# Kernel optimization log

Measured on AMD Instinct MI355X. Metric: run time of the kernel, lower is better.

## Reference

```python
import jax, jax.numpy as jnp
import numpy as np

H, DI, N, K, R, FF = 2048, 4096, 16, 4, 128, 5632
B, S = 2, 1024
EPS = 1e-6


def rmsnorm(x, w):
    v = jnp.mean(x * x, axis=-1, keepdims=True)
    return x * jax.lax.rsqrt(v + EPS) * w


def setup_inputs() -> dict:
    key = jax.random.key(0)
    ks = jax.random.split(key, 16)
    sc = 0.02
    inp = {
        "hidden_states": jax.random.normal(ks[0], (B, S, H), jnp.float32),
        "input_ln_w": jnp.ones((H,), jnp.float32),
        "w_in": jax.random.normal(ks[1], (2 * DI, H), jnp.float32) * sc,
        "conv_w": jax.random.normal(ks[2], (DI, 1, K), jnp.float32) * 0.3,
        "conv_b": jax.random.normal(ks[3], (DI,), jnp.float32) * sc,
        "w_x": jax.random.normal(ks[4], (R + 2 * N, DI), jnp.float32) * sc,
        "dt_ln_w": jnp.ones((R,), jnp.float32),
        "b_ln_w": jnp.ones((N,), jnp.float32),
        "c_ln_w": jnp.ones((N,), jnp.float32),
        "w_dt": jax.random.normal(ks[5], (DI, R), jnp.float32) * sc,
        "b_dt": jax.random.normal(ks[6], (DI,), jnp.float32) * sc - 4.0,
        "A_log": jnp.broadcast_to(jnp.log(jnp.arange(1, N + 1, dtype=jnp.float32)), (DI, N)),
        "D_skip": jnp.ones((DI,), jnp.float32),
        "w_out": jax.random.normal(ks[7], (H, DI), jnp.float32) * sc,
        "pre_ff_ln_w": jnp.ones((H,), jnp.float32),
        "w_gate": jax.random.normal(ks[8], (FF, H), jnp.float32) * sc,
        "w_up": jax.random.normal(ks[9], (FF, H), jnp.float32) * sc,
        "w_down": jax.random.normal(ks[10], (H, FF), jnp.float32) * sc,
    }
    return inp


def causal_conv1d(x, w, b):
    # x: [B,S,DI], w: [DI,1,K] depthwise, left-pad K-1 (causal)
    y = jax.lax.conv_general_dilated(
        x.transpose(0, 2, 1), w,
        window_strides=(1,), padding=[(K - 1, 0)],
        dimension_numbers=("NCH", "OIH", "NCH"),
        feature_group_count=DI)
    return (y + b[None, :, None]).transpose(0, 2, 1)


def selective_scan(u, A, Bm, Cm, Dp, dt):
    # u,dt: [B,S,DI]; A: [DI,N]; Bm,Cm: [B,S,N]
    def step(h, xs):
        dt_t, B_t, C_t, u_t = xs  # [B,DI],[B,N],[B,N],[B,DI]
        dA = jnp.exp(dt_t[:, :, None] * A)                      # [B,DI,N]
        dBu = dt_t[:, :, None] * B_t[:, None, :] * u_t[:, :, None]
        h = dA * h + dBu
        y = jnp.einsum("bdn,bn->bd", h, C_t)
        return h, y

    xs = (dt.transpose(1, 0, 2), Bm.transpose(1, 0, 2),
          Cm.transpose(1, 0, 2), u.transpose(1, 0, 2))
    h0 = jnp.zeros((u.shape[0], DI, N), u.dtype)
    _, ys = jax.lax.scan(step, h0, xs)
    return ys.transpose(1, 0, 2) + u * Dp  # [B,S,DI]


def reference(hidden_states, input_ln_w, w_in, conv_w, conv_b, w_x, dt_ln_w,
              b_ln_w, c_ln_w, w_dt, b_dt, A_log, D_skip, w_out, pre_ff_ln_w,
              w_gate, w_up, w_down):
    residual = hidden_states
    x = rmsnorm(hidden_states, input_ln_w)

    # --- Mamba mixer ---
    proj = x @ w_in.T                       # [B,S,2*DI]
    u, gate = jnp.split(proj, 2, axis=-1)
    u = jax.nn.silu(causal_conv1d(u, conv_w, conv_b))
    ssm_p = u @ w_x.T                       # [B,S,R+2N]
    t_r, Bm, Cm = jnp.split(ssm_p, [R, R + N], axis=-1)
    t_r = rmsnorm(t_r, dt_ln_w)
    Bm = rmsnorm(Bm, b_ln_w)
    Cm = rmsnorm(Cm, c_ln_w)
    dt = jax.nn.softplus(t_r @ w_dt.T + b_dt)  # [B,S,DI]
    A = -jnp.exp(A_log)
    y = selective_scan(u, A, Bm, Cm, D_skip, dt)
    y = y * jax.nn.silu(gate)
    mixer_out = y @ w_out.T                  # [B,S,H]

    hidden = residual + mixer_out
    residual = hidden
    h = rmsnorm(hidden, pre_ff_ln_w)
    ff = (jax.nn.silu(h @ w_gate.T) * (h @ w_up.T)) @ w_down.T
    return residual + ff
```

## Files before the change

### kernel.cpp

```cpp
#include <hip/hip_runtime.h>
#include <stdint.h>

#define H_   2048
#define DI_  4096
#define N_   16
#define K_   4
#define R_   128
#define FF_  5632
#define B_   2
#define S_   1024
#define MROWS (B_*S_)
#define PCH  32
#define CSTEPS (S_/PCH)

typedef float f32x4 __attribute__((ext_vector_type(4)));
typedef float f32x2 __attribute__((ext_vector_type(2)));
typedef __bf16 bf16x8 __attribute__((ext_vector_type(8)));

#define LOG2E 1.4426950408889634f
#define LN2   0.6931471805599453f

__device__ __forceinline__ unsigned short f2bf(float f) {
    union { float f; unsigned u; } v; v.f = f;
    unsigned r = v.u + 0x7fffu + ((v.u >> 16) & 1u);
    return (unsigned short)(r >> 16);
}

__device__ __forceinline__ float bf2f(unsigned short u) {
    union { unsigned u; float f; } v; v.u = ((unsigned)u) << 16;
    return v.f;
}

__device__ __forceinline__ float fexp2(float x) { return __builtin_amdgcn_exp2f(x); }
__device__ __forceinline__ float flog2(float x) { return __builtin_amdgcn_logf(x); }

__device__ __forceinline__ float softplus2(float v) {
    return (v > 20.f) ? v : LN2 * flog2(1.f + fexp2(v * LOG2E));
}

__device__ __forceinline__ void gload16(const void* g, void* lds) {
    __builtin_amdgcn_global_load_lds(
        (const __attribute__((address_space(1))) unsigned int*)(uintptr_t)g,
        (__attribute__((address_space(3))) unsigned int*)(unsigned int)(uintptr_t)lds,
        16, 0, 0);
}

__global__ __launch_bounds__(256, 2)
void gemm_bt(const unsigned short* __restrict__ A, const unsigned short* __restrict__ Bt,
             void* __restrict__ Cv, int M, int N, int K, int Kc, int obf)
{
    __shared__ __align__(16) unsigned short As[128 * 64];
    __shared__ __align__(16) unsigned short Bs[128 * 64];
    const int t = threadIdx.x;
    const int l = t & 63;
    const int wv = t >> 6;

    int nwg = gridDim.x * gridDim.y;
    int wg = blockIdx.y * gridDim.x + blockIdx.x;
    if ((nwg & 7) == 0) {
        int q = nwg >> 3;
        wg = (wg & 7) * q + (wg >> 3);
    }
    const int bx = wg / gridDim.y;
    const int by = wg % gridDim.y;
    const long m0 = (long)by * 128;
    const long n0 = (long)bx * 128;
    const int wm = (wv >> 1) * 64;
    const int wn = (wv & 1) * 64;
    const long kstart = (long)blockIdx.z * Kc;
    const long cbase = (long)blockIdx.z * M * (long)N;

    f32x4 acc[4][4] = {};

    const int tr = t >> 3;
    const int cs = (t & 7) ^ (tr & 7);
    const unsigned short* gA = A + (m0 + tr) * (long)K + kstart + cs * 8;
    const unsigned short* gB = Bt + (n0 + tr) * (long)K + kstart + cs * 8;
    const unsigned ldsbase = (unsigned)(t & 192) * 16;

    for (int kt = 0; kt < Kc; kt += 64) {
#pragma unroll
        for (int j = 0; j < 4; ++j) {
            gload16(gA + (long)j * 32 * K, (char*)As + j * 4096 + ldsbase);
            gload16(gB + (long)j * 32 * K, (char*)Bs + j * 4096 + ldsbase);
        }
        gA += 64; gB += 64;
        __syncthreads();
#pragma unroll
        for (int k0 = 0; k0 < 2; ++k0) {
            bf16x8 af[4], bfr[4];
#pragma unroll
            for (int i = 0; i < 4; ++i) {
                int rowa = wm + i * 16 + (l & 15);
                int ca = (k0 * 4 + (l >> 4)) ^ (rowa & 7);
                af[i] = *(const bf16x8*)(As + rowa * 64 + ca * 8);
                int rowb = wn + i * 16 + (l & 15);
                int cb = (k0 * 4 + (l >> 4)) ^ (rowb & 7);
                bfr[i] = *(const bf16x8*)(Bs + rowb * 64 + cb * 8);
            }
#pragma unroll
            for (int i = 0; i < 4; ++i)
#pragma unroll
                for (int jn = 0; jn < 4; ++jn)
                    acc[i][jn] = __builtin_amdgcn_mfma_f32_16x16x32_bf16(
                        af[i], bfr[jn], acc[i][jn], 0, 0, 0);
        }
        __syncthreads();
    }

    const int crow = (l >> 4) * 4;
    const int ccol = l & 15;
    float* Cf = (float*)Cv + cbase;
    unsigned short* Cb = (unsigned short*)Cv + cbase;
#pragma unroll
    for (int i = 0; i < 4; ++i) {
#pragma unroll
        for (int jn = 0; jn < 4; ++jn) {
            long row = m0 + wm + i * 16 + crow;
            long col = n0 + wn + jn * 16 + ccol;
            if (obf) {
                unsigned short* cp = Cb + row * (long)N + col;
#pragma unroll
                for (int q = 0; q < 4; ++q) cp[(long)q * N] = f2bf(acc[i][jn][q]);
            } else {
                float* cp = Cf + row * (long)N + col;
#pragma unroll
                for (int q = 0; q < 4; ++q) cp[(long)q * N] = acc[i][jn][q];
            }
        }
    }
}

__global__ __launch_bounds__(512, 1)
void gemm_bt256(const unsigned short* __restrict__ A, const unsigned short* __restrict__ Bt,
                void* __restrict__ Cv, int M, int N, int K, int Kc, int obf)
{
    __shared__ __align__(16) unsigned short As[2][256 * 64];
    __shared__ __align__(16) unsigned short Bs[2][256 * 64];
    const int t = threadIdx.x;
    const int l = t & 63;
    const int wv = t >> 6;
    const int wm = wv >> 2;
    const int wn = wv & 3;

    int nwg = gridDim.x * gridDim.y;
    int wg = blockIdx.y * gridDim.x + blockIdx.x;
    if ((nwg & 7) == 0) {
        int q = nwg >> 3;
        wg = (wg & 7) * q + (wg >> 3);
    }
    const int bx = wg / gridDim.y;
    const int by = wg % gridDim.y;
    const long m0 = (long)by * 256;
    const long n0 = (long)bx * 256;
    const long kstart = (long)blockIdx.z * Kc;
    const long cbase = (long)blockIdx.z * M * (long)N;

    f32x4 acc[8][4] = {};

    const int cs = (t & 7) ^ ((t >> 3) & 7);
    const unsigned short* gA = A + (m0 + (t >> 3)) * (long)K + kstart + cs * 8;
    const unsigned short* gB = Bt + (n0 + (t >> 3)) * (long)K + kstart + cs * 8;
    const int NT = Kc >> 6;

#pragma unroll
    for (int i = 0; i < 4; ++i)
        gload16(gA + (long)i * 64 * K, &As[0][t * 8 + i * 4096]);
#pragma unroll
    for (int i = 0; i < 4; ++i)
        gload16(gB + (long)i * 64 * K, &Bs[0][t * 8 + i * 4096]);

    for (int kt = 0; kt < NT; ++kt) {
        const int buf = kt & 1;
        const long koff = (long)((kt + 1 < NT) ? (kt + 1) : kt) * 64;
#pragma unroll
        for (int i = 0; i < 4; ++i)
            gload16(gA + koff + (long)i * 64 * K, &As[buf ^ 1][t * 8 + i * 4096]);
        asm volatile("s_waitcnt vmcnt(4)" ::: "memory");
        __builtin_amdgcn_sched_barrier(0);
        __builtin_amdgcn_s_barrier();
        __builtin_amdgcn_sched_barrier(0);
        {
            bf16x8 af[8], bfr[4];
#pragma unroll
            for (int nf = 0; nf < 4; ++nf) {
                int rowb = wn * 64 + nf * 16 + (l & 15);
                int cb = (l >> 4) ^ (rowb & 7);
                bfr[nf] = *(const bf16x8*)(&Bs[buf][rowb * 64 + cb * 8]);
            }
#pragma unroll
            for (int mf = 0; mf < 8; ++mf) {
                int rowa = wm * 128 + mf * 16 + (l & 15);
                int ca = (l >> 4) ^ (rowa & 7);
                af[mf] = *(const bf16x8*)(&As[buf][rowa * 64 + ca * 8]);
            }
            __builtin_amdgcn_s_setprio(1);
#pragma unroll
            for (int mf = 0; mf < 8; ++mf)
#pragma unroll
                for (int nf = 0; nf < 4; ++nf)
                    acc[mf][nf] = __builtin_amdgcn_mfma_f32_16x16x32_bf16(
                        af[mf], bfr[nf], acc[mf][nf], 0, 0, 0);
            __builtin_amdgcn_s_setprio(0);
        }
        __builtin_amdgcn_sched_barrier(0);
#pragma unroll
        for (int i = 0; i < 4; ++i)
            gload16(gB + koff + (long)i * 64 * K, &Bs[buf ^ 1][t * 8 + i * 4096]);
        {
            bf16x8 af[8], bfr[4];
#pragma unroll
            for (int nf = 0; nf < 4; ++nf) {
                int rowb = wn * 64 + nf * 16 + (l & 15);
                int cb = (4 + (l >> 4)) ^ (rowb & 7);
                bfr[nf] = *(const bf16x8*)(&Bs[buf][rowb * 64 + cb * 8]);
            }
#pragma unroll
            for (int mf = 0; mf < 8; ++mf) {
                int rowa = wm * 128 + mf * 16 + (l & 15);
                int ca = (4 + (l >> 4)) ^ (rowa & 7);
                af[mf] = *(const bf16x8*)(&As[buf][rowa * 64 + ca * 8]);
            }
            __builtin_amdgcn_s_setprio(1);
#pragma unroll
            for (int mf = 0; mf < 8; ++mf)
#pragma unroll
                for (int nf = 0; nf < 4; ++nf)
                    acc[mf][nf] = __builtin_amdgcn_mfma_f32_16x16x32_bf16(
                        af[mf], bfr[nf], acc[mf][nf], 0, 0, 0);
            __builtin_amdgcn_s_setprio(0);
        }
        __builtin_amdgcn_sched_barrier(0);
        __builtin_amdgcn_s_barrier();
        __builtin_amdgcn_sched_barrier(0);
    }

    const int crow = (l >> 4) * 4;
    const int ccol = l & 15;
    float* Cf = (float*)Cv + cbase;
    unsigned short* Cb = (unsigned short*)Cv + cbase;
#pragma unroll
    for (int mf = 0; mf < 8; ++mf) {
#pragma unroll
        for (int nf = 0; nf < 4; ++nf) {
            long row = m0 + wm * 128 + mf * 16 + crow;
            long col = n0 + wn * 64 + nf * 16 + ccol;
            if (obf) {
                unsigned short* cp = Cb + row * (long)N + col;
#pragma unroll
                for (int q = 0; q < 4; ++q) cp[(long)q * N] = f2bf(acc[mf][nf][q]);
            } else {
                float* cp = Cf + row * (long)N + col;
#pragma unroll
                for (int q = 0; q < 4; ++q) cp[(long)q * N] = acc[mf][nf][q];
            }
        }
    }
}

__global__ __launch_bounds__(256)
void cvt_bf16(const float* __restrict__ x, unsigned short* __restrict__ y, long n)
{
    long i = ((long)blockIdx.x * 256 + threadIdx.x) * 4;
    if (i >= n) return;
    float4 v = *(const float4*)(x + i);
    ushort4 o;
    o.x = f2bf(v.x); o.y = f2bf(v.y); o.z = f2bf(v.z); o.w = f2bf(v.w);
    *(ushort4*)(y + i) = o;
}

__global__ __launch_bounds__(256)
void cvt_pad_wx(const float* __restrict__ x, unsigned short* __restrict__ y)
{
    long i = ((long)blockIdx.x * 256 + threadIdx.x) * 4;
    int row = (int)(i >> 12);
    ushort4 o;
    if (row < 160) {
        float4 v = *(const float4*)(x + i);
        o.x = f2bf(v.x); o.y = f2bf(v.y); o.z = f2bf(v.z); o.w = f2bf(v.w);
    } else { o.x = 0; o.y = 0; o.z = 0; o.w = 0; }
    *(ushort4*)(y + i) = o;
}

__global__ __launch_bounds__(256)
void rmsnorm_cast(const float* __restrict__ x, const float* __restrict__ w,
                  unsigned short* __restrict__ out)
{
    const long row = blockIdx.x;
    const float* xr = x + row * H_ + threadIdx.x * 8;
    float4 v0 = *(const float4*)xr;
    float4 v1 = *(const float4*)(xr + 4);
    float xv[8] = {v0.x, v0.y, v0.z, v0.w, v1.x, v1.y, v1.z, v1.w};
    float s = 0.f;
#pragma unroll
    for (int j = 0; j < 8; ++j) s += xv[j] * xv[j];
#pragma unroll
    for (int m = 32; m; m >>= 1) s += __shfl_xor(s, m);
    __shared__ float red[4];
    if ((threadIdx.x & 63) == 0) red[threadIdx.x >> 6] = s;
    __syncthreads();
    s = red[0] + red[1] + red[2] + red[3];
    float inv = rsqrtf(s * (1.f / H_) + 1e-6f);
    const float* wr = w + threadIdx.x * 8;
    unsigned short* op = out + row * H_ + threadIdx.x * 8;
    ushort4 o0, o1;
    o0.x = f2bf(xv[0] * inv * wr[0]); o0.y = f2bf(xv[1] * inv * wr[1]);
    o0.z = f2bf(xv[2] * inv * wr[2]); o0.w = f2bf(xv[3] * inv * wr[3]);
    o1.x = f2bf(xv[4] * inv * wr[4]); o1.y = f2bf(xv[5] * inv * wr[5]);
    o1.z = f2bf(xv[6] * inv * wr[6]); o1.w = f2bf(xv[7] * inv * wr[7]);
    *(ushort4*)op = o0;
    *(ushort4*)(op + 4) = o1;
}

__global__ __launch_bounds__(256)
void add_rmsnorm(const float* __restrict__ a, const unsigned short* __restrict__ mx,
                 const float* __restrict__ w, float* __restrict__ hid,
                 unsigned short* __restrict__ hb)
{
    const long row = blockIdx.x;
    const long off = row * H_ + threadIdx.x * 8;
    float xv[8];
    {
        float4 a0 = *(const float4*)(a + off);
        float4 a1 = *(const float4*)(a + off + 4);
        xv[0] = a0.x; xv[1] = a0.y; xv[2] = a0.z; xv[3] = a0.w;
        xv[4] = a1.x; xv[5] = a1.y; xv[6] = a1.z; xv[7] = a1.w;
    }
#pragma unroll
    for (int z = 0; z < 4; ++z) {
        const unsigned short* mz = mx + (long)z * MROWS * H_ + off;
        ushort4 b0 = *(const ushort4*)mz;
        ushort4 b1 = *(const ushort4*)(mz + 4);
        xv[0] += bf2f(b0.x); xv[1] += bf2f(b0.y); xv[2] += bf2f(b0.z); xv[3] += bf2f(b0.w);
        xv[4] += bf2f(b1.x); xv[5] += bf2f(b1.y); xv[6] += bf2f(b1.z); xv[7] += bf2f(b1.w);
    }
    float s = 0.f;
#pragma unroll
    for (int j = 0; j < 8; ++j) s += xv[j] * xv[j];
#pragma unroll
    for (int m = 32; m; m >>= 1) s += __shfl_xor(s, m);
    __shared__ float red[4];
    if ((threadIdx.x & 63) == 0) red[threadIdx.x >> 6] = s;
    __syncthreads();
    s = red[0] + red[1] + red[2] + red[3];
    float inv = rsqrtf(s * (1.f / H_) + 1e-6f);
    float4 h0, h1;
    h0.x = xv[0]; h0.y = xv[1]; h0.z = xv[2]; h0.w = xv[3];
    h1.x = xv[4]; h1.y = xv[5]; h1.z = xv[6]; h1.w = xv[7];
    *(float4*)(hid + off) = h0;
    *(float4*)(hid + off + 4) = h1;
    const float* wr = w + threadIdx.x * 8;
    ushort4 o0, o1;
    o0.x = f2bf(xv[0] * inv * wr[0]); o0.y = f2bf(xv[1] * inv * wr[1]);
    o0.z = f2bf(xv[2] * inv * wr[2]); o0.w = f2bf(xv[3] * inv * wr[3]);
    o1.x = f2bf(xv[4] * inv * wr[4]); o1.y = f2bf(xv[5] * inv * wr[5]);
    o1.z = f2bf(xv[6] * inv * wr[6]); o1.w = f2bf(xv[7] * inv * wr[7]);
    *(ushort4*)(hb + off) = o0;
    *(ushort4*)(hb + off + 4) = o1;
}

__global__ __launch_bounds__(256)
void conv_silu(const unsigned short* __restrict__ proj, const float* __restrict__ cw,
               const float* __restrict__ cb, unsigned short* __restrict__ ub)
{
    long i = ((long)blockIdx.x * 256 + threadIdx.x) * 4;
    int d = (int)(i & (DI_ - 1));
    long sd = i >> 12;
    int s = (int)(sd & (S_ - 1));
    long rb = sd * (2 * DI_) + d;
    ushort4 x0 = *(const ushort4*)(proj + rb);
    ushort4 x1 = {0, 0, 0, 0}, x2 = {0, 0, 0, 0}, x3 = {0, 0, 0, 0};
    if (s >= 1) x1 = *(const ushort4*)(proj + rb - 2 * DI_);
    if (s >= 2) x2 = *(const ushort4*)(proj + rb - 4 * DI_);
    if (s >= 3) x3 = *(const ushort4*)(proj + rb - 6 * DI_);
    float4 bias = *(const float4*)(cb + d);
    unsigned short xs0[4] = {x0.x, x0.y, x0.z, x0.w};
    unsigned short xs1[4] = {x1.x, x1.y, x1.z, x1.w};
    unsigned short xs2[4] = {x2.x, x2.y, x2.z, x2.w};
    unsigned short xs3[4] = {x3.x, x3.y, x3.z, x3.w};
    float bs[4] = {bias.x, bias.y, bias.z, bias.w};
    unsigned short os[4];
#pragma unroll
    for (int j = 0; j < 4; ++j) {
        float4 wj = *(const float4*)(cw + (d + j) * 4);
        float acc = bs[j] + wj.w * bf2f(xs0[j]);
        if (s >= 1) acc += wj.z * bf2f(xs1[j]);
        if (s >= 2) acc += wj.y * bf2f(xs2[j]);
        if (s >= 3) acc += wj.x * bf2f(xs3[j]);
        float r = acc / (1.f + __expf(-acc));
        os[j] = f2bf(r);
    }
    ushort4 o; o.x = os[0]; o.y = os[1]; o.z = os[2]; o.w = os[3];
    *(ushort4*)(ub + i) = o;
}

__global__ __launch_bounds__(256)
void ssm_norms(const unsigned short* __restrict__ ssmp, const float* __restrict__ wdt,
               const float* __restrict__ wb, const float* __restrict__ wc,
               unsigned short* __restrict__ trb, float* __restrict__ Bm,
               float* __restrict__ Cm)
{
    const long row = (long)blockIdx.x * 4 + (threadIdx.x >> 6);
    const int l = threadIdx.x & 63;
    float x0 = 0.f, x1 = 0.f, xb = 0.f, xc = 0.f;
#pragma unroll
    for (int z = 0; z < 8; ++z) {
        const unsigned short* rp = ssmp + (long)z * (MROWS * 256) + row * 256;
        x0 += bf2f(rp[l]);
        x1 += bf2f(rp[64 + l]);
        xb += bf2f(rp[128 + (l & 15)]);
        xc += bf2f(rp[144 + (l & 15)]);
    }
    float s = x0 * x0 + x1 * x1;
#pragma unroll
    for (int m = 32; m; m >>= 1) s += __shfl_xor(s, m);
    float inv = rsqrtf(s * (1.f / R_) + 1e-6f);
    trb[row * R_ + l] = f2bf(x0 * inv * wdt[l]);
    trb[row * R_ + 64 + l] = f2bf(x1 * inv * wdt[64 + l]);

    float sb = xb * xb, sc = xc * xc;
#pragma unroll
    for (int m = 8; m; m >>= 1) { sb += __shfl_xor(sb, m); sc += __shfl_xor(sc, m); }
    float invb = rsqrtf(sb * (1.f / N_) + 1e-6f);
    float invc = rsqrtf(sc * (1.f / N_) + 1e-6f);
    if (l < 16) {
        Bm[row * N_ + l] = xb * invb * wb[l];
        Cm[row * N_ + l] = xc * invc * wc[l];
    }
}


__global__ __launch_bounds__(256)
void scan_partA(const unsigned short* __restrict__ ub, const unsigned short* __restrict__ dtraw,
                const float* __restrict__ bdt, const float* __restrict__ Bm,
                const float* __restrict__ A_log,
                float* __restrict__ TRH, float* __restrict__ TRS)
{
    const int w = __builtin_amdgcn_readfirstlane(threadIdx.x >> 6);
    const int l = threadIdx.x & 63;
    const int task = blockIdx.x * 4 + w;
    const int dchunk = task >> 5;
    const int p = task & 31;
    const int gch0 = dchunk * 64;
    const int batch = gch0 >> 12;
    const int d0 = gch0 & (DI_ - 1);
    const int d = d0 + l;
    const long bS = (long)batch * S_;
    const int t0 = p * CSTEPS;

    float Av2[16];
#pragma unroll
    for (int n = 0; n < 16; ++n)
        Av2[n] = -fexp2(A_log[(long)d * N_ + n] * LOG2E) * LOG2E;
    const float bias = bdt[d];

    float h[16];
#pragma unroll
    for (int n = 0; n < 16; ++n) h[n] = 0.f;
    float sdt = 0.f;

    float uN = bf2f(ub[(bS + t0) * DI_ + d]);
    float tN = bf2f(dtraw[(bS + t0) * DI_ + d]);
    float BN[16];
    {
        const float* Bp = Bm + (bS + t0) * N_;
#pragma unroll
        for (int n = 0; n < 16; ++n) BN[n] = Bp[n];
    }

    for (int s = 0; s < CSTEPS; ++s) {
        float uC = uN, tC = tN;
        float BC[16];
#pragma unroll
        for (int n = 0; n < 16; ++n) BC[n] = BN[n];
        if (s + 1 < CSTEPS) {
            long r2 = bS + t0 + s + 1;
            uN = bf2f(ub[r2 * DI_ + d]);
            tN = bf2f(dtraw[r2 * DI_ + d]);
            const float* Bp = Bm + r2 * N_;
#pragma unroll
            for (int n = 0; n < 16; ++n) BN[n] = Bp[n];
        }
        float dt = softplus2(tC + bias);
        float dtu = dt * uC;
        sdt += dt;
#pragma unroll
        for (int n = 0; n < 16; ++n) {
            float e = fexp2(dt * Av2[n]);
            h[n] = fmaf(e, h[n], dtu * BC[n]);
        }
    }
    float* hp = &TRH[(long)(gch0 + l) * (PCH * 16) + p * 16];
#pragma unroll
    for (int n = 0; n < 16; ++n) hp[n] = h[n];
    TRS[(long)(gch0 + l) * PCH + p] = sdt;
}

__global__ __launch_bounds__(256)
void scan_combine(const float* __restrict__ A_log, const float* __restrict__ TRS,
                  float* __restrict__ TRH)
{
    const int tid = blockIdx.x * 256 + threadIdx.x;
    const int gch = tid >> 4, n = tid & 15;
    const int d = gch & (DI_ - 1);
    const float Av = -__expf(A_log[(long)d * N_ + n]);
    const float* sp = TRS + (long)gch * PCH;
    float* hp = TRH + (long)gch * (PCH * 16) + n;
    float h = 0.f;
#pragma unroll
    for (int p = 0; p < PCH; ++p) {
        float hl = hp[p * 16];
        float e = __expf(Av * sp[p]);
        hp[p * 16] = h;
        h = hl + e * h;
    }
}

__global__ __launch_bounds__(256)
void scan_partC(const unsigned short* __restrict__ ub, const unsigned short* __restrict__ dtraw,
                const float* __restrict__ bdt, const float* __restrict__ Bm,
                const float* __restrict__ Cm, const float* __restrict__ A_log,
                const float* __restrict__ Dskip, const unsigned short* __restrict__ proj,
                const float* __restrict__ TRH, unsigned short* __restrict__ yb)
{
    const int w = __builtin_amdgcn_readfirstlane(threadIdx.x >> 6);
    const int l = threadIdx.x & 63;
    const int task = blockIdx.x * 4 + w;
    const int dchunk = task >> 5;
    const int p = task & 31;
    const int gch0 = dchunk * 64;
    const int batch = gch0 >> 12;
    const int d0 = gch0 & (DI_ - 1);
    const int d = d0 + l;
    const long bS = (long)batch * S_;
    const int t0 = p * CSTEPS;

    float Av2[16];
#pragma unroll
    for (int n = 0; n < 16; ++n)
        Av2[n] = -fexp2(A_log[(long)d * N_ + n] * LOG2E) * LOG2E;
    const float bias = bdt[d];
    const float Dv = Dskip[d];

    float h[16];
    {
        const float* hp = &TRH[(long)(gch0 + l) * (PCH * 16) + p * 16];
#pragma unroll
        for (int n = 0; n < 16; ++n) h[n] = hp[n];
    }

    float uN = bf2f(ub[(bS + t0) * DI_ + d]);
    float tN = bf2f(dtraw[(bS + t0) * DI_ + d]);
    float gN = bf2f(proj[(bS + t0) * (2L * DI_) + DI_ + d]);
    float BN[16], CN[16];
    {
        const float* Bp = Bm + (bS + t0) * N_;
        const float* Cp = Cm + (bS + t0) * N_;
#pragma unroll
        for (int n = 0; n < 16; ++n) { BN[n] = Bp[n]; CN[n] = Cp[n]; }
    }

    for (int s = 0; s < CSTEPS; ++s) {
        float uC = uN, tC = tN, gC = gN;
        float BC[16], CC_[16];
#pragma unroll
        for (int n = 0; n < 16; ++n) { BC[n] = BN[n]; CC_[n] = CN[n]; }
        if (s + 1 < CSTEPS) {
            long r2 = bS + t0 + s + 1;
            uN = bf2f(ub[r2 * DI_ + d]);
            tN = bf2f(dtraw[r2 * DI_ + d]);
            gN = bf2f(proj[r2 * (2L * DI_) + DI_ + d]);
            const float* Bp = Bm + r2 * N_;
            const float* Cp = Cm + r2 * N_;
#pragma unroll
            for (int n = 0; n < 16; ++n) { BN[n] = Bp[n]; CN[n] = Cp[n]; }
        }
        float dt = softplus2(tC + bias);
        float dtu = dt * uC;
        float y = uC * Dv;
#pragma unroll
        for (int n = 0; n < 16; ++n) {
            float e = fexp2(dt * Av2[n]);
            h[n] = fmaf(e, h[n], dtu * BC[n]);
            y = fmaf(h[n], CC_[n], y);
        }
        float eg = fexp2(-gC * LOG2E);
        float sl = gC * __builtin_amdgcn_rcpf(1.f + eg);
        yb[(bS + t0 + s) * DI_ + d] = f2bf(y * sl);
    }
}

__global__ __launch_bounds__(256)
void silu_mul2(const unsigned short* __restrict__ gfu, unsigned short* __restrict__ out,
               long n)
{
    long i = ((long)blockIdx.x * 256 + threadIdx.x) * 4;
    if (i >= n) return;
    long m = i / FF_;
    int f = (int)(i - m * FF_);
    const long NW = 2L * FF_;
    const unsigned short* r0 = gfu + m * NW;
    const unsigned short* r1 = gfu + (long)MROWS * NW + m * NW;
    ushort4 g0 = *(const ushort4*)(r0 + f);
    ushort4 g1 = *(const ushort4*)(r1 + f);
    ushort4 u0 = *(const ushort4*)(r0 + FF_ + f);
    ushort4 u1 = *(const ushort4*)(r1 + FF_ + f);
    float gv[4] = {bf2f(g0.x) + bf2f(g1.x), bf2f(g0.y) + bf2f(g1.y),
                   bf2f(g0.z) + bf2f(g1.z), bf2f(g0.w) + bf2f(g1.w)};
    float uv[4] = {bf2f(u0.x) + bf2f(u1.x), bf2f(u0.y) + bf2f(u1.y),
                   bf2f(u0.z) + bf2f(u1.z), bf2f(u0.w) + bf2f(u1.w)};
    unsigned short os[4];
#pragma unroll
    for (int j = 0; j < 4; ++j)
        os[j] = f2bf(gv[j] / (1.f + __expf(-gv[j])) * uv[j]);
    ushort4 o; o.x = os[0]; o.y = os[1]; o.z = os[2]; o.w = os[3];
    *(ushort4*)(out + i) = o;
}

__global__ __launch_bounds__(256)
void final_add(const float* __restrict__ a, const unsigned short* __restrict__ b,
               float* __restrict__ y, long n)
{
    long i = ((long)blockIdx.x * 256 + threadIdx.x) * 4;
    if (i >= n) return;
    float4 av = *(const float4*)(a + i);
    float4 o = av;
#pragma unroll
    for (int z = 0; z < 4; ++z) {
        ushort4 bv = *(const ushort4*)(b + (long)z * MROWS * H_ + i);
        o.x += bf2f(bv.x); o.y += bf2f(bv.y); o.z += bf2f(bv.z); o.w += bf2f(bv.w);
    }
    *(float4*)(y + i) = o;
}

extern "C" void kernel_launch(void* const* d_in, const int* in_sizes, int n_in,
                              void* d_out, int out_size, void* d_ws, size_t ws_size,
                              hipStream_t stream)
{
    const float* hs     = (const float*)d_in[0];
    const float* ln_in  = (const float*)d_in[1];
    const float* w_in   = (const float*)d_in[2];
    const float* conv_w = (const float*)d_in[3];
    const float* conv_b = (const float*)d_in[4];
    const float* w_x    = (const float*)d_in[5];
    const float* dt_ln  = (const float*)d_in[6];
    const float* b_ln   = (const float*)d_in[7];
    const float* c_ln   = (const float*)d_in[8];
    const float* w_dt   = (const float*)d_in[9];
    const float* b_dt   = (const float*)d_in[10];
    const float* A_log  = (const float*)d_in[11];
    const float* Dskip  = (const float*)d_in[12];
    const float* w_out  = (const float*)d_in[13];
    const float* ln_ff  = (const float*)d_in[14];
    const float* w_gate = (const float*)d_in[15];
    const float* w_up   = (const float*)d_in[16];
    const float* w_down = (const float*)d_in[17];
    float* out = (float*)d_out;
    char* ws = (char*)d_ws;

    unsigned short* WB    = (unsigned short*)(ws + 0L);
    unsigned short* XB    = (unsigned short*)(ws + 33554432L);
    unsigned short* PROJ  = (unsigned short*)(ws + 41943040L);
    unsigned short* MIX   = (unsigned short*)(ws + 41943040L);
    unsigned short* GFU   = (unsigned short*)(ws + 41943040L);
    unsigned short* FFT   = (unsigned short*)(ws + 41943040L);
    unsigned short* UB    = (unsigned short*)(ws + 142606336L);
    float*          HID   = (float*)(ws + 142606336L);
    unsigned short* TRB   = (unsigned short*)(ws + 159383552L);
    float*          BM    = (float*)(ws + 159907840L);
    float*          CM    = (float*)(ws + 160038912L);
    float*          TRS   = (float*)(ws + 160169984L);
    unsigned short* SSMP  = (unsigned short*)(ws + 161218560L);
    unsigned short* DTRAW = (unsigned short*)(ws + 161218560L);
    unsigned short* FFACT = (unsigned short*)(ws + 161218560L);
    float*          TRH   = (float*)(ws + 194772992L);
    unsigned short* WGU   = (unsigned short*)(ws + 194772992L);
    unsigned short* YB    = (unsigned short*)(ws + 227803136L);
    unsigned short* HB    = XB;

    auto gemm = [&](const unsigned short* A, const unsigned short* Bt, void* C,
                    int M, int N, int K, int kch, int obf) {
        dim3 g(N / 128, M / 128, kch);
        gemm_bt<<<g, 256, 0, stream>>>(A, Bt, C, M, N, K, K / kch, obf);
    };
    auto gemm256 = [&](const unsigned short* A, const unsigned short* Bt, void* C,
                       int M, int N, int K, int kch, int obf) {
        dim3 g(N / 256, M / 256, kch);
        gemm_bt256<<<g, 512, 0, stream>>>(A, Bt, C, M, N, K, K / kch, obf);
    };
    auto cvt = [&](const float* x, unsigned short* y, long n) {
        cvt_bf16<<<(int)((n / 4 + 255) / 256), 256, 0, stream>>>(x, y, n);
    };

    cvt(w_in, WB, (long)2 * DI_ * H_);
    rmsnorm_cast<<<MROWS, 256, 0, stream>>>(hs, ln_in, XB);
    gemm256(XB, WB, PROJ, MROWS, 2 * DI_, H_, 1, 1);
    conv_silu<<<(MROWS * DI_ / 4) / 256, 256, 0, stream>>>(PROJ, conv_w, conv_b, UB);
    cvt_pad_wx<<<(256 * DI_ / 4) / 256, 256, 0, stream>>>(w_x, WB);
    gemm(UB, WB, SSMP, MROWS, 256, DI_, 8, 1);
    ssm_norms<<<MROWS / 4, 256, 0, stream>>>(SSMP, dt_ln, b_ln, c_ln, TRB, BM, CM);
    cvt(w_dt, WB, (long)DI_ * R_);
    gemm(TRB, WB, DTRAW, MROWS, DI_, R_, 1, 1);
    scan_partA<<<(B_ * DI_ / 64) * PCH / 4, 256, 0, stream>>>(UB, DTRAW, b_dt, BM,
                                                              A_log, TRH, TRS);
    scan_combine<<<(B_ * DI_ * N_) / 256, 256, 0, stream>>>(A_log, TRS, TRH);
    scan_partC<<<(B_ * DI_ / 64) * PCH / 4, 256, 0, stream>>>(UB, DTRAW, b_dt, BM, CM,
                                                              A_log, Dskip, PROJ, TRH, YB);
    cvt(w_out, WB, (long)H_ * DI_);
    gemm256(YB, WB, MIX, MROWS, H_, DI_, 4, 1);
    add_rmsnorm<<<MROWS, 256, 0, stream>>>(hs, MIX, ln_ff, HID, HB);
    cvt(w_gate, WGU, (long)FF_ * H_);
    cvt(w_up, WGU + (long)FF_ * H_, (long)FF_ * H_);
    gemm256(HB, WGU, GFU, MROWS, 2 * FF_, H_, 2, 1);
    silu_mul2<<<(int)(((long)MROWS * FF_ / 4 + 255) / 256), 256, 0, stream>>>(
        GFU, FFACT, (long)MROWS * FF_);
    cvt(w_down, WB, (long)H_ * FF_);
    gemm256(FFACT, WB, FFT, MROWS, H_, FF_, 4, 1);
    final_add<<<(int)(((long)MROWS * H_ / 4 + 255) / 256), 256, 0, stream>>>(
        HID, FFT, out, (long)MROWS * H_);
}
```

Baseline: 482.4 us.

## Restructure GEMM main loop into four-quadrant ping-pong with staggered quarter-tile prefetch

Rewrites the bf16 MFMA GEMM inner loop so each wave computes its 128x64 output in four quadrants. Each quadrant loads its LDS fragments, issues a quarter of the next tiles' global-to-LDS loads, and then runs its MFMAs. Prefetch now reaches two K-steps ahead for parts of A and B, and the stage loads are reorganised per wave with a new swizzle. The goal is to interleave memory traffic with MFMA work more finely and cut register pressure from fragments. In exchange it adds many more barriers per iteration and makes buffer-reuse correctness depend on delicate timing.

```diff
diff --git a/kernel.cpp b/kernel.cpp
--- a/kernel.cpp
+++ b/kernel.cpp
@@ -157,79 +157,150 @@
     const long cbase = (long)blockIdx.z * M * (long)N;
 
     f32x4 acc[8][4] = {};
-
-    const int cs = (t & 7) ^ ((t >> 3) & 7);
-    const unsigned short* gA = A + (m0 + (t >> 3)) * (long)K + kstart + cs * 8;
-    const unsigned short* gB = Bt + (n0 + (t >> 3)) * (long)K + kstart + cs * 8;
     const int NT = Kc >> 6;
-
-#pragma unroll
-    for (int i = 0; i < 4; ++i)
-        gload16(gA + (long)i * 64 * K, &As[0][t * 8 + i * 4096]);
-#pragma unroll
-    for (int i = 0; i < 4; ++i)
-        gload16(gB + (long)i * 64 * K, &Bs[0][t * 8 + i * 4096]);
+    const int cs8 = (l & 7) ^ (l >> 3);
+
+    auto stageA = [&](int qa, int kt2, int bufi) {
+#pragma unroll
+        for (int i = 0; i < 2; ++i) {
+            const int r16 = wv * 2 + i;
+            const int base_row = ((r16 >> 3) << 7) + (qa << 6) + ((r16 & 7) << 3);
+            gload16(A + (m0 + base_row + (l >> 3)) * (long)K + kstart + (long)kt2 * 64 + cs8 * 8,
+                    &As[bufi][base_row * 64 + l * 8]);
+        }
+    };
+    auto stageB = [&](int qb, int kt2, int bufi) {
+#pragma unroll
+        for (int i = 0; i < 2; ++i) {
+            const int r16 = wv * 2 + i;
+            const int base_row = ((r16 >> 2) << 6) + (qb << 5) + ((r16 & 3) << 3);
+            gload16(Bt + (n0 + base_row + (l >> 3)) * (long)K + kstart + (long)kt2 * 64 + cs8 * 8,
+                    &Bs[bufi][base_row * 64 + l * 8]);
+        }
+    };
+
+    stageA(0, 0, 0); stageB(1, 0, 0); stageA(1, 0, 0); stageB(0, 0, 0);
+    stageA(0, 1, 1); stageB(1, 1, 1); stageA(1, 1, 1);
+    asm volatile("s_waitcnt vmcnt(6)" ::: "memory");
+    __builtin_amdgcn_sched_barrier(0);
+    __builtin_amdgcn_s_barrier();
+    __builtin_amdgcn_sched_barrier(0);
 
     for (int kt = 0; kt < NT; ++kt) {
-        const int buf = kt & 1;
-        const long koff = (long)((kt + 1 < NT) ? (kt + 1) : kt) * 64;
-#pragma unroll
-        for (int i = 0; i < 4; ++i)
-            gload16(gA + koff + (long)i * 64 * K, &As[buf ^ 1][t * 8 + i * 4096]);
+        const int buf = kt & 1, obuf = buf ^ 1;
+        const int kn1 = (kt + 1 < NT) ? kt + 1 : kt;
+        const int kn2 = (kt + 2 < NT) ? kt + 2 : NT - 1;
+        bf16x8 afq[4][2], bfq[2][2];
+
+#pragma unroll
+        for (int m2 = 0; m2 < 4; ++m2)
+#pragma unroll
+            for (int ks = 0; ks < 2; ++ks) {
+                int rowa = wm * 128 + m2 * 16 + (l & 15);
+                int ca = (ks * 4 + (l >> 4)) ^ (rowa & 7);
+                afq[m2][ks] = *(const bf16x8*)(&As[buf][rowa * 64 + ca * 8]);
+            }
+#pragma unroll
+        for (int n2 = 0; n2 < 2; ++n2)
+#pragma unroll
+            for (int ks = 0; ks < 2; ++ks) {
+                int rowb = wn * 64 + n2 * 16 + (l & 15);
+                int cb = (ks * 4 + (l >> 4)) ^ (rowb & 7);
+                bfq[n2][ks] = *(const bf16x8*)(&Bs[buf][rowb * 64 + cb * 8]);
+            }
+        stageB(0, kn1, obuf);
+        __builtin_amdgcn_s_barrier();
+        asm volatile("s_waitcnt lgkmcnt(0)" ::: "memory");
+        __builtin_amdgcn_sched_barrier(0);
+        __builtin_amdgcn_s_setprio(1);
+#pragma unroll
+        for (int m2 = 0; m2 < 4; ++m2)
+#pragma unroll
+            for (int n2 = 0; n2 < 2; ++n2)
+#pragma unroll
+                for (int ks = 0; ks < 2; ++ks)
+                    acc[m2][n2] = __builtin_amdgcn_mfma_f32_16x16x32_bf16(
+                        afq[m2][ks], bfq[n2][ks], acc[m2][n2], 0, 0, 0);
+        __builtin_amdgcn_s_setprio(0);
+        __builtin_amdgcn_sched_barrier(0);
+        __builtin_amdgcn_s_barrier();
+        __builtin_amdgcn_sched_barrier(0);
+
+#pragma unroll
+        for (int n2 = 0; n2 < 2; ++n2)
+#pragma unroll
+            for (int ks = 0; ks < 2; ++ks) {
+                int rowb = wn * 64 + (2 + n2) * 16 + (l & 15);
+                int cb = (ks * 4 + (l >> 4)) ^ (rowb & 7);
+                bfq[n2][ks] = *(const bf16x8*)(&Bs[buf][rowb * 64 + cb * 8]);
+            }
+        stageA(0, kn2, buf);
+        __builtin_amdgcn_s_barrier();
+        asm volatile("s_waitcnt lgkmcnt(0)" ::: "memory");
+        __builtin_amdgcn_sched_barrier(0);
+        __builtin_amdgcn_s_setprio(1);
+#pragma unroll
+        for (int m2 = 0; m2 < 4; ++m2)
+#pragma unroll
+            for (int n2 = 0; n2 < 2; ++n2)
+#pragma unroll
+                for (int ks = 0; ks < 2; ++ks)
+                    acc[m2][2 + n2] = __builtin_amdgcn_mfma_f32_16x16x32_bf16(
+                        afq[m2][ks], bfq[n2][ks], acc[m2][2 + n2], 0, 0, 0);
+        __builtin_amdgcn_s_setprio(0);
+        __builtin_amdgcn_sched_barrier(0);
+        __builtin_amdgcn_s_barrier();
+        __builtin_amdgcn_sched_barrier(0);
+
+#pragma unroll
+        for (int m2 = 0; m2 < 4; ++m2)
+#pragma unroll
+            for (int ks = 0; ks < 2; ++ks) {
+                int rowa = wm * 128 + (4 + m2) * 16 + (l & 15);
+                int ca = (ks * 4 + (l >> 4)) ^ (rowa & 7);
+                afq[m2][ks] = *(const bf16x8*)(&As[buf][rowa * 64 + ca * 8]);
+            }
+        stageB(1, kn2, buf);
+        __builtin_amdgcn_s_barrier();
+        asm volatile("s_waitcnt lgkmcnt(0)" ::: "memory");
+        __builtin_amdgcn_sched_barrier(0);
+        __builtin_amdgcn_s_setprio(1);
+#pragma unroll
+        for (int m2 = 0; m2 < 4; ++m2)
+#pragma unroll
+            for (int n2 = 0; n2 < 2; ++n2)
+#pragma unroll
+                for (int ks = 0; ks < 2; ++ks)
+                    acc[4 + m2][2 + n2] = __builtin_amdgcn_mfma_f32_16x16x32_bf16(
+                        afq[m2][ks], bfq[n2][ks], acc[4 + m2][2 + n2], 0, 0, 0);
+        __builtin_amdgcn_s_setprio(0);
+        __builtin_amdgcn_sched_barrier(0);
+        __builtin_amdgcn_s_barrier();
+        __builtin_amdgcn_sched_barrier(0);
+
+#pragma unroll
+        for (int n2 = 0; n2 < 2; ++n2)
+#pragma unroll
+            for (int ks = 0; ks < 2; ++ks) {
+                int rowb = wn * 64 + n2 * 16 + (l & 15);
+                int cb = (ks * 4 + (l >> 4)) ^ (rowb & 7);
+                bfq[n2][ks] = *(const bf16x8*)(&Bs[buf][rowb * 64 + cb * 8]);
+            }
+        stageA(1, kn2, buf);
+        __builtin_amdgcn_s_barrier();
+        asm volatile("s_waitcnt lgkmcnt(0)" ::: "memory");
+        __builtin_amdgcn_sched_barrier(0);
+        __builtin_amdgcn_s_setprio(1);
+#pragma unroll
+        for (int m2 = 0; m2 < 4; ++m2)
+#pragma unroll
+            for (int n2 = 0; n2 < 2; ++n2)
+#pragma unroll
+                for (int ks = 0; ks < 2; ++ks)
+                    acc[4 + m2][n2] = __builtin_amdgcn_mfma_f32_16x16x32_bf16(
+                        afq[m2][ks], bfq[n2][ks], acc[4 + m2][n2], 0, 0, 0);
+        __builtin_amdgcn_s_setprio(0);
         asm volatile("s_waitcnt vmcnt(4)" ::: "memory");
-        __builtin_amdgcn_sched_barrier(0);
-        __builtin_amdgcn_s_barrier();
-        __builtin_amdgcn_sched_barrier(0);
-        {
-            bf16x8 af[8], bfr[4];
-#pragma unroll
-            for (int nf = 0; nf < 4; ++nf) {
-                int rowb = wn * 64 + nf * 16 + (l & 15);
-                int cb = (l >> 4) ^ (rowb & 7);
-                bfr[nf] = *(const bf16x8*)(&Bs[buf][rowb * 64 + cb * 8]);
-            }
-#pragma unroll
-            for (int mf = 0; mf < 8; ++mf) {
-                int rowa = wm * 128 + mf * 16 + (l & 15);
-                int ca = (l >> 4) ^ (rowa & 7);
-                af[mf] = *(const bf16x8*)(&As[buf][rowa * 64 + ca * 8]);
-            }
-            __builtin_amdgcn_s_setprio(1);
-#pragma unroll
-            for (int mf = 0; mf < 8; ++mf)
-#pragma unroll
-                for (int nf = 0; nf < 4; ++nf)
-                    acc[mf][nf] = __builtin_amdgcn_mfma_f32_16x16x32_bf16(
-                        af[mf], bfr[nf], acc[mf][nf], 0, 0, 0);
-            __builtin_amdgcn_s_setprio(0);
-        }
-        __builtin_amdgcn_sched_barrier(0);
-#pragma unroll
-        for (int i = 0; i < 4; ++i)
-            gload16(gB + koff + (long)i * 64 * K, &Bs[buf ^ 1][t * 8 + i * 4096]);
-        {
-            bf16x8 af[8], bfr[4];
-#pragma unroll
-            for (int nf = 0; nf < 4; ++nf) {
-                int rowb = wn * 64 + nf * 16 + (l & 15);
-                int cb = (4 + (l >> 4)) ^ (rowb & 7);
-                bfr[nf] = *(const bf16x8*)(&Bs[buf][rowb * 64 + cb * 8]);
-            }
-#pragma unroll
-            for (int mf = 0; mf < 8; ++mf) {
-                int rowa = wm * 128 + mf * 16 + (l & 15);
-                int ca = (4 + (l >> 4)) ^ (rowa & 7);
-                af[mf] = *(const bf16x8*)(&As[buf][rowa * 64 + ca * 8]);
-            }
-            __builtin_amdgcn_s_setprio(1);
-#pragma unroll
-            for (int mf = 0; mf < 8; ++mf)
-#pragma unroll
-                for (int nf = 0; nf < 4; ++nf)
-                    acc[mf][nf] = __builtin_amdgcn_mfma_f32_16x16x32_bf16(
-                        af[mf], bfr[nf], acc[mf][nf], 0, 0, 0);
-            __builtin_amdgcn_s_setprio(0);
-        }
         __builtin_amdgcn_sched_barrier(0);
         __builtin_amdgcn_s_barrier();
         __builtin_amdgcn_sched_barrier(0);
```

After: 489.5 us. About the same (+1.5%).
